# Kernel tuning notes

Hardware: AMD Instinct MI355X
Metric: run time of the kernel (lower is better)

Reference implementation:

```python
import jax, jax.numpy as jnp
import numpy as np

B, N, D, S, ITERS, EPS = 32, 4096, 512, 8, 3, 1e-8


def layer_norm(x, g, b, eps=1e-5):
    mu = jnp.mean(x, axis=-1, keepdims=True)
    var = jnp.var(x, axis=-1, keepdims=True)
    return (x - mu) * jax.lax.rsqrt(var + eps) * g + b


def setup_inputs() -> dict:
    key = jax.random.key(0)
    ks = jax.random.split(key, 12)
    sc = 1.0 / np.sqrt(D)
    return {
        "inputs": jax.random.normal(ks[0], (B, N, D), jnp.float32),
        "noise": jax.random.normal(ks[1], (B, S, D), jnp.float32),
        "slots_mu": jax.random.normal(ks[2], (1, S, D), jnp.float32),
        "slots_sigma": jnp.ones((1, S, D), jnp.float32),
        "ln_in_g": jnp.ones((D,), jnp.float32), "ln_in_b": jnp.zeros((D,), jnp.float32),
        "ln_s_g": jnp.ones((D,), jnp.float32), "ln_s_b": jnp.zeros((D,), jnp.float32),
        "wq": jax.random.normal(ks[3], (D, D), jnp.float32) * sc,
        "wk": jax.random.normal(ks[4], (D, D), jnp.float32) * sc,
        "wv": jax.random.normal(ks[5], (D, D), jnp.float32) * sc,
        "w_ih": jax.random.normal(ks[6], (3 * D, D), jnp.float32) * sc,
        "w_hh": jax.random.normal(ks[7], (3 * D, D), jnp.float32) * sc,
        "b_ih": jnp.zeros((3 * D,), jnp.float32),
        "b_hh": jnp.zeros((3 * D,), jnp.float32),
        "ln_m_g": jnp.ones((D,), jnp.float32), "ln_m_b": jnp.zeros((D,), jnp.float32),
        "w1": jax.random.normal(ks[8], (D, D), jnp.float32) * sc,
        "b1": jnp.zeros((D,), jnp.float32),
        "w2": jax.random.normal(ks[9], (D, D), jnp.float32) * sc,
        "b2": jnp.zeros((D,), jnp.float32),
    }


def reference(inputs, noise, slots_mu, slots_sigma, ln_in_g, ln_in_b, ln_s_g, ln_s_b,
              wq, wk, wv, w_ih, w_hh, b_ih, b_hh, ln_m_g, ln_m_b, w1, b1, w2, b2):
    # slot init: mu + sigma * N(0,1)
    slots = slots_mu + slots_sigma * noise          # (B,S,D)
    x = layer_norm(inputs, ln_in_g, ln_in_b)        # (B,N,D)
    k = jnp.einsum('bnd,ed->bne', x, wk)            # (B,N,D)
    v = jnp.einsum('bnd,ed->bne', x, wv)            # (B,N,D)
    for _ in range(ITERS):
        slots_prev = slots
        sn = layer_norm(slots, ln_s_g, ln_s_b)
        q = jnp.einsum('bsd,ed->bse', sn, wq)       # (B,S,D)
        logits = jnp.einsum('bnd,bsd->bns', k, q)   # (B,N,S)
        attn = jax.nn.softmax(logits, axis=-1) + EPS  # softmax over slots
        attn = attn / jnp.sum(attn, axis=-1, keepdims=True)
        attn_t = jnp.swapaxes(attn, -1, -2)         # (B,S,N)
        updates = jnp.einsum('bsn,bnd->bsd', attn_t, v)
        # GRUCell(input=updates, hidden=slots_prev)
        gi = jnp.einsum('bsd,ed->bse', updates, w_ih) + b_ih
        gh = jnp.einsum('bsd,ed->bse', slots_prev, w_hh) + b_hh
        gi_r, gi_z, gi_n = jnp.split(gi, 3, axis=-1)
        gh_r, gh_z, gh_n = jnp.split(gh, 3, axis=-1)
        r = jax.nn.sigmoid(gi_r + gh_r)
        z = jax.nn.sigmoid(gi_z + gh_z)
        n = jnp.tanh(gi_n + r * gh_n)
        slots = (1.0 - z) * n + z * slots_prev
        # residual MLP
        h = layer_norm(slots, ln_m_g, ln_m_b)
        h = jax.nn.relu(jnp.einsum('bsd,ed->bse', h, w1) + b1)
        slots = slots + jnp.einsum('bsd,ed->bse', h, w2) + b2
    return slots
```

## Files before the change

### kernel.cpp

```cpp
#include <hip/hip_runtime.h>

#define B_ 32
#define N_ 4096
#define D_ 512
#define S_ 8
#define ITERS_ 3

__device__ __forceinline__ float sigmoid_f(float x) {
    return 1.0f / (1.0f + __expf(-x));
}
__device__ __forceinline__ float tanh_f(float x) {
    float e = __expf(2.0f * x);
    return 1.0f - 2.0f / (e + 1.0f);
}

__global__ __launch_bounds__(256) void k_init(const float* __restrict__ noise,
                                              const float* __restrict__ mu,
                                              const float* __restrict__ sg,
                                              float* __restrict__ slots,
                                              float* __restrict__ stats) {
    int wid = threadIdx.x >> 6, lane = threadIdx.x & 63;
    int row = blockIdx.x * 4 + wid;
    const float4* nz = (const float4*)(noise + (size_t)row * D_);
    const float4* m4 = (const float4*)(mu + (size_t)(row & 7) * D_);
    const float4* s4 = (const float4*)(sg + (size_t)(row & 7) * D_);
    float4 v0 = nz[lane], v1 = nz[64 + lane];
    float4 a0 = m4[lane], a1 = m4[64 + lane];
    float4 c0 = s4[lane], c1 = s4[64 + lane];
    v0.x = fmaf(c0.x, v0.x, a0.x); v0.y = fmaf(c0.y, v0.y, a0.y);
    v0.z = fmaf(c0.z, v0.z, a0.z); v0.w = fmaf(c0.w, v0.w, a0.w);
    v1.x = fmaf(c1.x, v1.x, a1.x); v1.y = fmaf(c1.y, v1.y, a1.y);
    v1.z = fmaf(c1.z, v1.z, a1.z); v1.w = fmaf(c1.w, v1.w, a1.w);
    float4* o4 = (float4*)(slots + (size_t)row * D_);
    o4[lane] = v0; o4[64 + lane] = v1;
    float s1 = v0.x + v0.y + v0.z + v0.w + v1.x + v1.y + v1.z + v1.w;
    float s2 = v0.x*v0.x; s2 = fmaf(v0.y,v0.y,s2); s2 = fmaf(v0.z,v0.z,s2); s2 = fmaf(v0.w,v0.w,s2);
    s2 = fmaf(v1.x,v1.x,s2); s2 = fmaf(v1.y,v1.y,s2); s2 = fmaf(v1.z,v1.z,s2); s2 = fmaf(v1.w,v1.w,s2);
#pragma unroll
    for (int off = 32; off > 0; off >>= 1) {
        s1 += __shfl_xor(s1, off, 64);
        s2 += __shfl_xor(s2, off, 64);
    }
    if (lane == 0) {
        float mean = s1 * (1.0f / D_);
        float var  = s2 * (1.0f / D_) - mean * mean;
        stats[row * 2]     = mean;
        stats[row * 2 + 1] = rsqrtf(var + 1e-5f);
    }
}

template<int WT, int LNA>
__global__ __launch_bounds__(256) void k_gemm(const float* __restrict__ A,
                                              const float* __restrict__ W,
                                              const float* __restrict__ bias,
                                              float* __restrict__ C,
                                              int M, int N, int K,
                                              const float* __restrict__ stats,
                                              const float* __restrict__ lng,
                                              const float* __restrict__ lnb) {
    __shared__ float As[64][68];
    __shared__ float Ws[64][36];
    int t  = threadIdx.x;
    int bm = blockIdx.y * 64, bn = blockIdx.x * 32;
    int tm = t >> 4, tn = t & 15;
    float acc[4][2] = {{0.f,0.f},{0.f,0.f},{0.f,0.f},{0.f,0.f}};

    for (int kk = 0; kk < K; kk += 64) {
        __syncthreads();
        if (WT == 2) {
#pragma unroll
            for (int r = 0; r < 4; ++r) {
                int idx = t + r * 256;
                int k = idx >> 4, m4 = idx & 15;
                float4 a4 = *(const float4*)(A + (size_t)(kk + k) * M + bm + (m4 << 2));
                *(float4*)&As[k][m4 << 2] = a4;
            }
        } else {
#pragma unroll
            for (int r = 0; r < 4; ++r) {
                int flat = t * 4 + r * 1024;
                int m = flat >> 6, k = flat & 63;
                float4 a4 = *(const float4*)(A + (size_t)(bm + m) * K + kk + k);
                if (LNA) {
                    float mean = stats[(bm + m) * 2];
                    float rs   = stats[(bm + m) * 2 + 1];
                    float4 g4 = *(const float4*)(lng + kk + k);
                    float4 b4 = *(const float4*)(lnb + kk + k);
                    a4.x = fmaf((a4.x - mean) * rs, g4.x, b4.x);
                    a4.y = fmaf((a4.y - mean) * rs, g4.y, b4.y);
                    a4.z = fmaf((a4.z - mean) * rs, g4.z, b4.z);
                    a4.w = fmaf((a4.w - mean) * rs, g4.w, b4.w);
                }
                As[k + 0][m] = a4.x; As[k + 1][m] = a4.y;
                As[k + 2][m] = a4.z; As[k + 3][m] = a4.w;
            }
        }
        if (WT == 1) {
#pragma unroll
            for (int r = 0; r < 2; ++r) {
                int flat = t * 4 + r * 1024;
                int n = flat >> 6, k = flat & 63;
                float4 w4 = *(const float4*)(W + (size_t)(bn + n) * K + kk + k);
                Ws[k + 0][n] = w4.x; Ws[k + 1][n] = w4.y;
                Ws[k + 2][n] = w4.z; Ws[k + 3][n] = w4.w;
            }
        } else {
#pragma unroll
            for (int r = 0; r < 2; ++r) {
                int flat = t * 4 + r * 1024;
                int k = flat >> 5, n = flat & 31;
                float4 w4 = *(const float4*)(W + (size_t)(kk + k) * N + bn + n);
                *(float4*)&Ws[k][n] = w4;
            }
        }
        __syncthreads();
#pragma unroll
        for (int k = 0; k < 64; ++k) {
            float4 a = *(const float4*)&As[k][tm << 2];
            float2 w = *(const float2*)&Ws[k][tn << 1];
            acc[0][0] = fmaf(a.x, w.x, acc[0][0]); acc[0][1] = fmaf(a.x, w.y, acc[0][1]);
            acc[1][0] = fmaf(a.y, w.x, acc[1][0]); acc[1][1] = fmaf(a.y, w.y, acc[1][1]);
            acc[2][0] = fmaf(a.z, w.x, acc[2][0]); acc[2][1] = fmaf(a.z, w.y, acc[2][1]);
            acc[3][0] = fmaf(a.w, w.x, acc[3][0]); acc[3][1] = fmaf(a.w, w.y, acc[3][1]);
        }
    }
#pragma unroll
    for (int i = 0; i < 4; ++i) {
#pragma unroll
        for (int j = 0; j < 2; ++j) {
            int row = bm + (tm << 2) + i;
            int col = bn + (tn << 1) + j;
            float v = acc[i][j];
            if (bias) v += bias[col];
            C[(size_t)row * N + col] = v;
        }
    }
}

__global__ __launch_bounds__(512, 2) void k_attn_gh(const float* __restrict__ x,
                                                    const float* __restrict__ qk,
                                                    const float* __restrict__ g,
                                                    const float* __restrict__ bvec,
                                                    float* __restrict__ part,
                                                    float* __restrict__ bsum,
                                                    const float* __restrict__ slots,
                                                    const float* __restrict__ w_hh,
                                                    const float* __restrict__ b_hh,
                                                    float* __restrict__ gg) {
    __shared__ float smem[8704];
    const int blk = blockIdx.x;
    const int t = threadIdx.x;

    if (blk >= 512) {
        const int t2 = blk - 512;
        const int ci = t2 % 24, ri = t2 / 24;
        const int bm = ri * 64, bn = ci * 64;
        float (*As)[68] = (float (*)[68])smem;
        float (*Ws)[68] = (float (*)[68])(smem + 64 * 68);
        const int tm = t >> 5, tn = t & 31;
        float acc[4][2] = {{0.f,0.f},{0.f,0.f},{0.f,0.f},{0.f,0.f}};
        for (int kk = 0; kk < 512; kk += 64) {
            __syncthreads();
#pragma unroll
            for (int r = 0; r < 2; ++r) {
                int flat = t * 4 + r * 2048;
                int m = flat >> 6, k = flat & 63;
                float4 a4 = *(const float4*)(slots + (size_t)(bm + m) * 512 + kk + k);
                As[k + 0][m] = a4.x; As[k + 1][m] = a4.y;
                As[k + 2][m] = a4.z; As[k + 3][m] = a4.w;
            }
#pragma unroll
            for (int r = 0; r < 2; ++r) {
                int flat = t * 4 + r * 2048;
                int n = flat >> 6, k = flat & 63;
                float4 w4 = *(const float4*)(w_hh + (size_t)(bn + n) * 512 + kk + k);
                Ws[k + 0][n] = w4.x; Ws[k + 1][n] = w4.y;
                Ws[k + 2][n] = w4.z; Ws[k + 3][n] = w4.w;
            }
            __syncthreads();
#pragma unroll
            for (int k = 0; k < 64; ++k) {
                const float4 a = *(const float4*)&As[k][tm << 2];
                const float2 w = *(const float2*)&Ws[k][tn << 1];
                acc[0][0] = fmaf(a.x, w.x, acc[0][0]); acc[0][1] = fmaf(a.x, w.y, acc[0][1]);
                acc[1][0] = fmaf(a.y, w.x, acc[1][0]); acc[1][1] = fmaf(a.y, w.y, acc[1][1]);
                acc[2][0] = fmaf(a.z, w.x, acc[2][0]); acc[2][1] = fmaf(a.z, w.y, acc[2][1]);
                acc[3][0] = fmaf(a.w, w.x, acc[3][0]); acc[3][1] = fmaf(a.w, w.y, acc[3][1]);
            }
        }
#pragma unroll
        for (int i = 0; i < 4; ++i) {
#pragma unroll
            for (int j = 0; j < 2; ++j) {
                int row = bm + (tm << 2) + i;
                int col = bn + (tn << 1) + j;
                gg[(size_t)row * 3072 + col] = acc[i][j] + b_hh[col];
            }
        }
        return;
    }

    float* qts  = smem;
    float* u0s  = smem + 4096;
    float* red  = smem + 8192;
    float* red2 = smem + 8256;
    float* c12  = smem + 8320;
    const int nc = blk & 15, b = blk >> 4;
    const int w = t >> 6, lane = t & 63;

    {
        const float4* qk4 = (const float4*)(qk + (size_t)b * 4096);
        const float4* g4 = (const float4*)g;
        const float4* b4 = (const float4*)bvec;
        float c1p[2], c2p[2];
#pragma unroll
        for (int r = 0; r < 2; ++r) {
            int f = t + r * 512;
            float4 v = qk4[f];
            float4 gg4 = g4[f & 127];
            float4 bb = b4[f & 127];
            float4 qv = make_float4(v.x*gg4.x, v.y*gg4.y, v.z*gg4.z, v.w*gg4.w);
            *(float4*)&qts[((f & 127) * 8 + (f >> 7)) * 4] = qv;
            c1p[r] = qv.x + qv.y + qv.z + qv.w;
            c2p[r] = bb.x*v.x + bb.y*v.y + bb.z*v.z + bb.w*v.w;
        }
#pragma unroll
        for (int off = 32; off > 0; off >>= 1) {
#pragma unroll
            for (int r = 0; r < 2; ++r) {
                c1p[r] += __shfl_xor(c1p[r], off, 64);
                c2p[r] += __shfl_xor(c2p[r], off, 64);
            }
        }
        if (lane == 0) {
            red[w * 2 + 0] = c1p[0]; red[w * 2 + 1] = c1p[1];
            red2[w * 2 + 0] = c2p[0]; red2[w * 2 + 1] = c2p[1];
        }
    }
    __syncthreads();
    if (t < 8) {
        int s = t;
        float v1, v2;
        if (s < 4) { v1 = red[4*s]       + red[4*s + 2];       v2 = red2[4*s]       + red2[4*s + 2]; }
        else       { v1 = red[4*(s-4)+1] + red[4*(s-4)+3];     v2 = red2[4*(s-4)+1] + red2[4*(s-4)+3]; }
        c12[s] = v1; c12[8 + s] = v2;
    }
    __syncthreads();

    float4 qa[8], qb[8];
#pragma unroll
    for (int s = 0; s < 8; ++s) {
        qa[s] = *(const float4*)&qts[(lane * 8 + s) * 4];
        qb[s] = *(const float4*)&qts[((64 + lane) * 8 + s) * 4];
    }
    const int gq = (lane >> 3) & 7;
    const float c1g = c12[gq], c2g = c12[8 + gq];
    const bool hb5 = (lane & 32) != 0, hb4 = (lane & 16) != 0, hb3 = (lane & 8) != 0;
    const int gbase = lane & 7;
    const float cnorm = 1.0f / (1.0f + 8.0f * 1e-8f);
    const float eadd  = 1e-8f * cnorm;

    float4 acc0[8], acc1[8];
#pragma unroll
    for (int s = 0; s < 8; ++s) {
        acc0[s] = make_float4(0.f, 0.f, 0.f, 0.f);
        acc1[s] = make_float4(0.f, 0.f, 0.f, 0.f);
    }
    float aS = 0.f, tS = 0.f;

    const float4* xr = (const float4*)(x + ((size_t)b * N_ + (size_t)nc * 256 + w * 32) * D_);
    float4 cur0 = xr[lane],       cur1 = xr[64 + lane];
    float4 cur2 = xr[128 + lane], cur3 = xr[192 + lane];

#define DOTS(X0, X1, R)                                                          \
    {                                                                            \
        sx[R] = (X0).x + (X0).y + (X0).z + (X0).w                                \
              + (X1).x + (X1).y + (X1).z + (X1).w;                               \
        float t_ = (X0).x*(X0).x;                                                \
        t_ = fmaf((X0).y,(X0).y,t_); t_ = fmaf((X0).z,(X0).z,t_);                \
        t_ = fmaf((X0).w,(X0).w,t_); t_ = fmaf((X1).x,(X1).x,t_);                \
        t_ = fmaf((X1).y,(X1).y,t_); t_ = fmaf((X1).z,(X1).z,t_);                \
        t_ = fmaf((X1).w,(X1).w,t_); sxx[R] = t_;                                \
        _Pragma("unroll")                                                        \
        for (int s = 0; s < 8; ++s) {                                            \
            float td = (X0).x * qa[s].x;                                         \
            td = fmaf((X0).y, qa[s].y, td); td = fmaf((X0).z, qa[s].z, td);      \
            td = fmaf((X0).w, qa[s].w, td);                                      \
            td = fmaf((X1).x, qb[s].x, td); td = fmaf((X1).y, qb[s].y, td);      \
            td = fmaf((X1).z, qb[s].z, td); td = fmaf((X1).w, qb[s].w, td);      \
            dd[R][s] = td;                                                       \
        }                                                                        \
    }

    for (int jp = 0; jp < 16; ++jp) {
        int jn = (jp < 15) ? (2 * jp + 2) : 30;
        float4 n0 = xr[jn * 128 + lane],       n1 = xr[jn * 128 + 64 + lane];
        float4 n2 = xr[(jn + 1) * 128 + lane], n3 = xr[(jn + 1) * 128 + 64 + lane];

        float sx[2], sxx[2], dd[2][8];
        DOTS(cur0, cur1, 0);
        DOTS(cur2, cur3, 1);

        float r4[2][4];
#pragma unroll
        for (int r = 0; r < 2; ++r) {
#pragma unroll
            for (int s = 0; s < 4; ++s) {
                float snd = hb5 ? dd[r][s] : dd[r][s + 4];
                float kp  = hb5 ? dd[r][s + 4] : dd[r][s];
                r4[r][s] = kp + __shfl_xor(snd, 32, 64);
            }
        }
        float r2v[2][2];
#pragma unroll
        for (int r = 0; r < 2; ++r) {
#pragma unroll
            for (int s = 0; s < 2; ++s) {
                float snd = hb4 ? r4[r][s] : r4[r][s + 2];
                float kp  = hb4 ? r4[r][s + 2] : r4[r][s];
                r2v[r][s] = kp + __shfl_xor(snd, 16, 64);
            }
        }
        float vv[2];
#pragma unroll
        for (int r = 0; r < 2; ++r) {
            float snd = hb3 ? r2v[r][0] : r2v[r][1];
            float kp  = hb3 ? r2v[r][1] : r2v[r][0];
            vv[r] = kp + __shfl_xor(snd, 8, 64);
        }
#pragma unroll
        for (int off = 4; off > 0; off >>= 1) {
#pragma unroll
            for (int r = 0; r < 2; ++r) vv[r] += __shfl_xor(vv[r], off, 64);
        }
#pragma unroll
        for (int off = 32; off > 0; off >>= 1) {
#pragma unroll
            for (int r = 0; r < 2; ++r) {
                sx[r]  += __shfl_xor(sx[r], off, 64);
                sxx[r] += __shfl_xor(sxx[r], off, 64);
            }
        }
        float mean[2], rsv[2], lg[2];
#pragma unroll
        for (int r = 0; r < 2; ++r) {
            mean[r] = sx[r] * (1.0f / D_);
            rsv[r]  = rsqrtf(sxx[r] * (1.0f / D_) - mean[r] * mean[r] + 1e-5f);
            lg[r]   = fmaf(rsv[r], vv[r], fmaf(-rsv[r] * mean[r], c1g, c2g));
        }
        float mx[2] = { lg[0], lg[1] };
#pragma unroll
        for (int r = 0; r < 2; ++r) {
            mx[r] = fmaxf(mx[r], __shfl_xor(mx[r], 8, 64));
            mx[r] = fmaxf(mx[r], __shfl_xor(mx[r], 16, 64));
            mx[r] = fmaxf(mx[r], __shfl_xor(mx[r], 32, 64));
        }
        float pv[2], ps[2];
#pragma unroll
        for (int r = 0; r < 2; ++r) { pv[r] = __expf(lg[r] - mx[r]); ps[r] = pv[r]; }
#pragma unroll
        for (int r = 0; r < 2; ++r) {
            ps[r] += __shfl_xor(ps[r], 8, 64);
            ps[r] += __shfl_xor(ps[r], 16, 64);
            ps[r] += __shfl_xor(ps[r], 32, 64);
        }
        float av[2], wv[2];
#pragma unroll
        for (int r = 0; r < 2; ++r) {
            av[r] = fmaf(pv[r], cnorm / ps[r], eadd);
            wv[r] = av[r] * rsv[r];
        }
        aS += av[0]; aS += av[1];
        tS = fmaf(wv[0], mean[0], tS);
        tS = fmaf(wv[1], mean[1], tS);
#pragma unroll
        for (int s = 0; s < 8; ++s) {
            float w0 = __shfl(wv[0], (s << 3) | gbase, 64);
            float w1 = __shfl(wv[1], (s << 3) | gbase, 64);
            acc0[s].x = fmaf(w0, cur0.x, acc0[s].x); acc0[s].y = fmaf(w0, cur0.y, acc0[s].y);
            acc0[s].z = fmaf(w0, cur0.z, acc0[s].z); acc0[s].w = fmaf(w0, cur0.w, acc0[s].w);
            acc1[s].x = fmaf(w0, cur1.x, acc1[s].x); acc1[s].y = fmaf(w0, cur1.y, acc1[s].y);
            acc1[s].z = fmaf(w0, cur1.z, acc1[s].z); acc1[s].w = fmaf(w0, cur1.w, acc1[s].w);
            acc0[s].x = fmaf(w1, cur2.x, acc0[s].x); acc0[s].y = fmaf(w1, cur2.y, acc0[s].y);
            acc0[s].z = fmaf(w1, cur2.z, acc0[s].z); acc0[s].w = fmaf(w1, cur2.w, acc0[s].w);
            acc1[s].x = fmaf(w1, cur3.x, acc1[s].x); acc1[s].y = fmaf(w1, cur3.y, acc1[s].y);
            acc1[s].z = fmaf(w1, cur3.z, acc1[s].z); acc1[s].w = fmaf(w1, cur3.w, acc1[s].w);
        }
        cur0 = n0; cur1 = n1; cur2 = n2; cur3 = n3;
    }
#undef DOTS

    if ((lane & 7) == 0) { red[w * 8 + gq] = aS; red2[w * 8 + gq] = tS; }
    for (int w2 = 0; w2 < 8; ++w2) {
        if (w == w2) {
#pragma unroll
            for (int s = 0; s < 8; ++s) {
                float* p0 = &u0s[s * 512 + (lane << 2)];
                float* p1 = p0 + 256;
                if (w2 == 0) {
                    *(float4*)p0 = acc0[s];
                    *(float4*)p1 = acc1[s];
                } else {
                    float4 v0 = *(float4*)p0;
                    v0.x += acc0[s].x; v0.y += acc0[s].y; v0.z += acc0[s].z; v0.w += acc0[s].w;
                    *(float4*)p0 = v0;
                    float4 v1 = *(float4*)p1;
                    v1.x += acc1[s].x; v1.y += acc1[s].y; v1.z += acc1[s].z; v1.w += acc1[s].w;
                    *(float4*)p1 = v1;
                }
            }
        }
        __syncthreads();
    }
    if (t < 16) {
        int s = t & 7;
        const float* src = (t < 8) ? red : red2;
        float v = 0.f;
#pragma unroll
        for (int w2 = 0; w2 < 8; ++w2) v += src[w2 * 8 + s];
        bsum[(size_t)(b * 16 + nc) * 16 + t] = v;
    }
    float4* d4 = (float4*)(part + (size_t)(b * 16 + nc) * 4096);
    const float4* s4 = (const float4*)u0s;
    d4[t] = s4[t];
    d4[t + 512] = s4[t + 512];
}

__global__ __launch_bounds__(512) void k_ured(const float* __restrict__ part,
                                              const float* __restrict__ bsum,
                                              const float* __restrict__ g,
                                              const float* __restrict__ bvec,
                                              float* __restrict__ u0) {
    const int bs = blockIdx.x;
    const int b = bs >> 3, s = bs & 7;
    const int d = threadIdx.x;
    float Av = 0.f, Tv = 0.f;
#pragma unroll
    for (int nc = 0; nc < 16; ++nc) {
        Av += bsum[(size_t)(b * 16 + nc) * 16 + s];
        Tv += bsum[(size_t)(b * 16 + nc) * 16 + 8 + s];
    }
    float p = 0.f;
#pragma unroll
    for (int nc = 0; nc < 16; ++nc)
        p += part[(size_t)(b * 16 + nc) * 4096 + s * 512 + d];
    u0[(size_t)bs * 512 + d] = fmaf(g[d], p - Tv, Av * bvec[d]);
}

__global__ __launch_bounds__(256) void k_gi(const float* __restrict__ u0,
                                            const float* __restrict__ Wiv,
                                            const float* __restrict__ b_ih,
                                            float* __restrict__ gg) {
    __shared__ float As[64][68];
    __shared__ float Ws[64][36];
    const int t = threadIdx.x;
    const int bn = blockIdx.x * 32;
    const int bm = blockIdx.y * 64;
    int tm = t >> 4, tn = t & 15;
    float acc[4][2] = {{0.f,0.f},{0.f,0.f},{0.f,0.f},{0.f,0.f}};

    for (int kk = 0; kk < 512; kk += 64) {
        __syncthreads();
#pragma unroll
        for (int r = 0; r < 4; ++r) {
            int flat = t * 4 + r * 1024;
            int m = flat >> 6, k = flat & 63;
            float4 a4 = *(const float4*)(u0 + (size_t)(bm + m) * 512 + kk + k);
            As[k + 0][m] = a4.x; As[k + 1][m] = a4.y;
            As[k + 2][m] = a4.z; As[k + 3][m] = a4.w;
        }
#pragma unroll
        for (int r = 0; r < 2; ++r) {
            int flat = t * 4 + r * 1024;
            int n = flat >> 6, k = flat & 63;
            float4 w4 = *(const float4*)(Wiv + (size_t)(bn + n) * 512 + kk + k);
            Ws[k + 0][n] = w4.x; Ws[k + 1][n] = w4.y;
            Ws[k + 2][n] = w4.z; Ws[k + 3][n] = w4.w;
        }
        __syncthreads();
#pragma unroll
        for (int k = 0; k < 64; ++k) {
            float4 a = *(const float4*)&As[k][tm << 2];
            float2 w = *(const float2*)&Ws[k][tn << 1];
            acc[0][0] = fmaf(a.x, w.x, acc[0][0]); acc[0][1] = fmaf(a.x, w.y, acc[0][1]);
            acc[1][0] = fmaf(a.y, w.x, acc[1][0]); acc[1][1] = fmaf(a.y, w.y, acc[1][1]);
            acc[2][0] = fmaf(a.z, w.x, acc[2][0]); acc[2][1] = fmaf(a.z, w.y, acc[2][1]);
            acc[3][0] = fmaf(a.w, w.x, acc[3][0]); acc[3][1] = fmaf(a.w, w.y, acc[3][1]);
        }
    }
#pragma unroll
    for (int i = 0; i < 4; ++i) {
#pragma unroll
        for (int j = 0; j < 2; ++j) {
            int row = bm + (tm << 2) + i;
            int cw  = bn + (tn << 1) + j;
            gg[(size_t)row * 3072 + 1536 + cw] = acc[i][j] + b_ih[cw];
        }
    }
}

__global__ __launch_bounds__(512) void k_p2(const float* __restrict__ gg,
                                            const float* __restrict__ slots,
                                            const float* __restrict__ w1, const float* __restrict__ b1,
                                            const float* __restrict__ w2, const float* __restrict__ b2,
                                            const float* __restrict__ wqkT,
                                            const float* __restrict__ ln_m_g, const float* __restrict__ ln_m_b,
                                            const float* __restrict__ ln_s_g, const float* __restrict__ ln_s_b,
                                            float* __restrict__ dst, float* __restrict__ qkout, int last) {
    __shared__ float s2s[2][512];
    __shared__ float t0s[2][512];
    __shared__ float hs[2][512];
    __shared__ float stat[4];
    const int t = threadIdx.x;
    const int wid = t >> 6, lane = t & 63;
    const int r0 = blockIdx.x * 2;

#pragma unroll
    for (int j = 0; j < 2; ++j) {
        int flat = t + j * 512;
        int r = flat >> 9, d = flat & 511;
        size_t row = r0 + r;
        const float* ghb = gg + row * 3072;
        const float* gib = ghb + 1536;
        float gir = gib[d], giz = gib[d + 512], gin = gib[d + 1024];
        float ghr = ghb[d], ghz = ghb[d + 512], ghn = ghb[d + 1024];
        float rr = sigmoid_f(gir + ghr);
        float zz = sigmoid_f(giz + ghz);
        float nn = tanh_f(fmaf(rr, ghn, gin));
        float sp = slots[row * 512 + d];
        s2s[r][d] = fmaf(1.0f - zz, nn, zz * sp);
    }
    __syncthreads();
    if (wid < 2) {
        const float4* sr = (const float4*)s2s[wid];
        float4 a = sr[lane], bq = sr[64 + lane];
        float s1 = a.x + a.y + a.z + a.w + bq.x + bq.y + bq.z + bq.w;
        float s2 = a.x*a.x; s2 = fmaf(a.y,a.y,s2); s2 = fmaf(a.z,a.z,s2); s2 = fmaf(a.w,a.w,s2);
        s2 = fmaf(bq.x,bq.x,s2); s2 = fmaf(bq.y,bq.y,s2); s2 = fmaf(bq.z,bq.z,s2); s2 = fmaf(bq.w,bq.w,s2);
#pragma unroll
        for (int off = 32; off > 0; off >>= 1) {
            s1 += __shfl_xor(s1, off, 64);
            s2 += __shfl_xor(s2, off, 64);
        }
        if (lane == 0) {
            float mean = s1 * (1.0f / D_);
            float var  = s2 * (1.0f / D_) - mean * mean;
            stat[wid * 2] = mean;
            stat[wid * 2 + 1] = rsqrtf(var + 1e-5f);
        }
    }
    __syncthreads();
#pragma unroll
    for (int j = 0; j < 2; ++j) {
        int flat = t + j * 512;
        int r = flat >> 9, d = flat & 511;
        t0s[r][d] = fmaf((s2s[r][d] - stat[r * 2]) * stat[r * 2 + 1], ln_m_g[d], ln_m_b[d]);
    }
    __syncthreads();
    {
        const int c = t;
        const float4* wr = (const float4*)(w1 + (size_t)c * 512);
        float a0 = 0.f, a1 = 0.f;
#pragma unroll 8
        for (int k4 = 0; k4 < 128; ++k4) {
            float4 w4 = wr[k4];
            float4 q0 = *(const float4*)&t0s[0][k4 << 2];
            float4 q1 = *(const float4*)&t0s[1][k4 << 2];
            a0 = fmaf(q0.x, w4.x, a0); a0 = fmaf(q0.y, w4.y, a0);
            a0 = fmaf(q0.z, w4.z, a0); a0 = fmaf(q0.w, w4.w, a0);
            a1 = fmaf(q1.x, w4.x, a1); a1 = fmaf(q1.y, w4.y, a1);
            a1 = fmaf(q1.z, w4.z, a1); a1 = fmaf(q1.w, w4.w, a1);
        }
        float bc = b1[c];
        hs[0][c] = fmaxf(a0 + bc, 0.f);
        hs[1][c] = fmaxf(a1 + bc, 0.f);
    }
    __syncthreads();
    {
        const int c = t;
        const float4* wr = (const float4*)(w2 + (size_t)c * 512);
        float a0 = 0.f, a1 = 0.f;
#pragma unroll 8
        for (int k4 = 0; k4 < 128; ++k4) {
            float4 w4 = wr[k4];
            float4 q0 = *(const float4*)&hs[0][k4 << 2];
            float4 q1 = *(const float4*)&hs[1][k4 << 2];
            a0 = fmaf(q0.x, w4.x, a0); a0 = fmaf(q0.y, w4.y, a0);
            a0 = fmaf(q0.z, w4.z, a0); a0 = fmaf(q0.w, w4.w, a0);
            a1 = fmaf(q1.x, w4.x, a1); a1 = fmaf(q1.y, w4.y, a1);
            a1 = fmaf(q1.z, w4.z, a1); a1 = fmaf(q1.w, w4.w, a1);
        }
        float bc = b2[c];
        float o0 = s2s[0][c] + a0 + bc;
        float o1 = s2s[1][c] + a1 + bc;
        dst[(size_t)r0 * 512 + c] = o0;
        dst[(size_t)(r0 + 1) * 512 + c] = o1;
        s2s[0][c] = o0;
        s2s[1][c] = o1;
    }
    if (last) return;
    __syncthreads();
    if (wid < 2) {
        const float4* sr = (const float4*)s2s[wid];
        float4 a = sr[lane], bq = sr[64 + lane];
        float s1 = a.x + a.y + a.z + a.w + bq.x + bq.y + bq.z + bq.w;
        float s2 = a.x*a.x; s2 = fmaf(a.y,a.y,s2); s2 = fmaf(a.z,a.z,s2); s2 = fmaf(a.w,a.w,s2);
        s2 = fmaf(bq.x,bq.x,s2); s2 = fmaf(bq.y,bq.y,s2); s2 = fmaf(bq.z,bq.z,s2); s2 = fmaf(bq.w,bq.w,s2);
#pragma unroll
        for (int off = 32; off > 0; off >>= 1) {
            s1 += __shfl_xor(s1, off, 64);
            s2 += __shfl_xor(s2, off, 64);
        }
        if (lane == 0) {
            float mean = s1 * (1.0f / D_);
            float var  = s2 * (1.0f / D_) - mean * mean;
            stat[wid * 2] = mean;
            stat[wid * 2 + 1] = rsqrtf(var + 1e-5f);
        }
    }
    __syncthreads();
#pragma unroll
    for (int j = 0; j < 2; ++j) {
        int flat = t + j * 512;
        int r = flat >> 9, d = flat & 511;
        t0s[r][d] = fmaf((s2s[r][d] - stat[r * 2]) * stat[r * 2 + 1], ln_s_g[d], ln_s_b[d]);
    }
    __syncthreads();
    {
        const int c = t;
        const float4* wr = (const float4*)(wqkT + (size_t)c * 512);
        float a0 = 0.f, a1 = 0.f;
#pragma unroll 8
        for (int k4 = 0; k4 < 128; ++k4) {
            float4 w4 = wr[k4];
            float4 q0 = *(const float4*)&t0s[0][k4 << 2];
            float4 q1 = *(const float4*)&t0s[1][k4 << 2];
            a0 = fmaf(q0.x, w4.x, a0); a0 = fmaf(q0.y, w4.y, a0);
            a0 = fmaf(q0.z, w4.z, a0); a0 = fmaf(q0.w, w4.w, a0);
            a1 = fmaf(q1.x, w4.x, a1); a1 = fmaf(q1.y, w4.y, a1);
            a1 = fmaf(q1.z, w4.z, a1); a1 = fmaf(q1.w, w4.w, a1);
        }
        qkout[(size_t)r0 * 512 + c] = a0;
        qkout[(size_t)(r0 + 1) * 512 + c] = a1;
    }
}

extern "C" void kernel_launch(void* const* d_in, const int* in_sizes, int n_in,
                              void* d_out, int out_size, void* d_ws, size_t ws_size,
                              hipStream_t stream) {
    const float* inputs  = (const float*)d_in[0];
    const float* noise   = (const float*)d_in[1];
    const float* mu      = (const float*)d_in[2];
    const float* sg      = (const float*)d_in[3];
    const float* ln_in_g = (const float*)d_in[4];
    const float* ln_in_b = (const float*)d_in[5];
    const float* ln_s_g  = (const float*)d_in[6];
    const float* ln_s_b  = (const float*)d_in[7];
    const float* wq      = (const float*)d_in[8];
    const float* wk      = (const float*)d_in[9];
    const float* wv      = (const float*)d_in[10];
    const float* w_ih    = (const float*)d_in[11];
    const float* w_hh    = (const float*)d_in[12];
    const float* b_ih    = (const float*)d_in[13];
    const float* b_hh    = (const float*)d_in[14];
    const float* ln_m_g  = (const float*)d_in[15];
    const float* ln_m_b  = (const float*)d_in[16];
    const float* w1      = (const float*)d_in[17];
    const float* b1      = (const float*)d_in[18];
    const float* w2      = (const float*)d_in[19];
    const float* b2      = (const float*)d_in[20];

    float* ws = (float*)d_ws;
    const size_t SLOT = (size_t)B_ * S_ * D_;
    size_t o = 0;
    float* slots = ws + o; o += SLOT;
    float* qk    = ws + o; o += SLOT;
    float* u0    = ws + o; o += SLOT;
    float* gg    = ws + o; o += (size_t)256 * 3072;
    float* Mqk   = ws + o; o += (size_t)D_ * D_;
    float* Wiv   = ws + o; o += (size_t)3 * D_ * D_;
    float* statsS= ws + o; o += 512;
    float* part  = ws + o; o += (size_t)16 * B_ * 4096;
    float* bsum  = ws + o; o += (size_t)B_ * 16 * 16;

    k_gemm<2,0><<<dim3(16, 8), 256, 0, stream>>>(wk, wq, nullptr, Mqk,
                                                 512, 512, 512, nullptr, nullptr, nullptr);
    k_gemm<0,0><<<dim3(16, 24), 256, 0, stream>>>(w_ih, wv, nullptr, Wiv,
                                                  1536, 512, 512, nullptr, nullptr, nullptr);
    k_init<<<64, 256, 0, stream>>>(noise, mu, sg, slots, statsS);
    k_gemm<1,1><<<dim3(16, 4), 256, 0, stream>>>(slots, Mqk, nullptr, qk,
                                                 256, 512, 512, statsS, ln_s_g, ln_s_b);

    for (int it = 0; it < ITERS_; ++it) {
        k_attn_gh<<<608, 512, 0, stream>>>(inputs, qk, ln_in_g, ln_in_b, part, bsum,
                                           slots, w_hh, b_hh, gg);
        k_ured<<<256, 512, 0, stream>>>(part, bsum, ln_in_g, ln_in_b, u0);
        k_gi<<<dim3(48, 4), 256, 0, stream>>>(u0, Wiv, b_ih, gg);
        int last = (it == ITERS_ - 1);
        float* dst = last ? (float*)d_out : slots;
        k_p2<<<128, 512, 0, stream>>>(gg, slots, w1, b1, w2, b2, Mqk,
                                      ln_m_g, ln_m_b, ln_s_g, ln_s_b, dst, qk, last);
    }
}
```

Before: 700.4 us.

## Merge prologue kernels, cache input LN stats, restructure attention softmax via shared memory

Three prologue launches (two weight-product GEMMs and slot init) are merged into one kernel with a block-index dispatch. The attention kernel computes per-row layer-norm mean/rstd on the first iteration only, stores them to a workspace buffer, and reloads them in later iterations, so the sum and sum-of-squares reductions are not recomputed. The per-row softmax is also moved from shuffle-based cross-lane work to a single wave reading logits from shared memory, with 4 rows per warp per block step and extra block barriers. This adds a small workspace buffer and more synchronisation in exchange for fewer shuffles and launches.

```diff
diff --git a/kernel.cpp b/kernel.cpp
--- a/kernel.cpp
+++ b/kernel.cpp
@@ -14,54 +14,17 @@
     return 1.0f - 2.0f / (e + 1.0f);
 }
 
-__global__ __launch_bounds__(256) void k_init(const float* __restrict__ noise,
-                                              const float* __restrict__ mu,
-                                              const float* __restrict__ sg,
-                                              float* __restrict__ slots,
-                                              float* __restrict__ stats) {
-    int wid = threadIdx.x >> 6, lane = threadIdx.x & 63;
-    int row = blockIdx.x * 4 + wid;
-    const float4* nz = (const float4*)(noise + (size_t)row * D_);
-    const float4* m4 = (const float4*)(mu + (size_t)(row & 7) * D_);
-    const float4* s4 = (const float4*)(sg + (size_t)(row & 7) * D_);
-    float4 v0 = nz[lane], v1 = nz[64 + lane];
-    float4 a0 = m4[lane], a1 = m4[64 + lane];
-    float4 c0 = s4[lane], c1 = s4[64 + lane];
-    v0.x = fmaf(c0.x, v0.x, a0.x); v0.y = fmaf(c0.y, v0.y, a0.y);
-    v0.z = fmaf(c0.z, v0.z, a0.z); v0.w = fmaf(c0.w, v0.w, a0.w);
-    v1.x = fmaf(c1.x, v1.x, a1.x); v1.y = fmaf(c1.y, v1.y, a1.y);
-    v1.z = fmaf(c1.z, v1.z, a1.z); v1.w = fmaf(c1.w, v1.w, a1.w);
-    float4* o4 = (float4*)(slots + (size_t)row * D_);
-    o4[lane] = v0; o4[64 + lane] = v1;
-    float s1 = v0.x + v0.y + v0.z + v0.w + v1.x + v1.y + v1.z + v1.w;
-    float s2 = v0.x*v0.x; s2 = fmaf(v0.y,v0.y,s2); s2 = fmaf(v0.z,v0.z,s2); s2 = fmaf(v0.w,v0.w,s2);
-    s2 = fmaf(v1.x,v1.x,s2); s2 = fmaf(v1.y,v1.y,s2); s2 = fmaf(v1.z,v1.z,s2); s2 = fmaf(v1.w,v1.w,s2);
-#pragma unroll
-    for (int off = 32; off > 0; off >>= 1) {
-        s1 += __shfl_xor(s1, off, 64);
-        s2 += __shfl_xor(s2, off, 64);
-    }
-    if (lane == 0) {
-        float mean = s1 * (1.0f / D_);
-        float var  = s2 * (1.0f / D_) - mean * mean;
-        stats[row * 2]     = mean;
-        stats[row * 2 + 1] = rsqrtf(var + 1e-5f);
-    }
-}
-
 template<int WT, int LNA>
-__global__ __launch_bounds__(256) void k_gemm(const float* __restrict__ A,
-                                              const float* __restrict__ W,
-                                              const float* __restrict__ bias,
-                                              float* __restrict__ C,
-                                              int M, int N, int K,
-                                              const float* __restrict__ stats,
-                                              const float* __restrict__ lng,
-                                              const float* __restrict__ lnb) {
-    __shared__ float As[64][68];
-    __shared__ float Ws[64][36];
+__device__ void gemm_body(const float* __restrict__ A, const float* __restrict__ W,
+                          const float* __restrict__ bias, float* __restrict__ C,
+                          int M, int N, int K, int bxi, int byi,
+                          const float* __restrict__ stats,
+                          const float* __restrict__ lng, const float* __restrict__ lnb,
+                          float* smem) {
+    float (*As)[68] = (float (*)[68])smem;
+    float (*Ws)[36] = (float (*)[36])(smem + 64 * 68);
     int t  = threadIdx.x;
-    int bm = blockIdx.y * 64, bn = blockIdx.x * 32;
+    int bm = byi * 64, bn = bxi * 32;
     int tm = t >> 4, tn = t & 15;
     float acc[4][2] = {{0.f,0.f},{0.f,0.f},{0.f,0.f},{0.f,0.f}};
 
@@ -137,12 +100,77 @@
     }
 }
 
+__device__ void init_body(const float* __restrict__ noise, const float* __restrict__ mu,
+                          const float* __restrict__ sg, float* __restrict__ slots,
+                          float* __restrict__ stats, int blk) {
+    int wid = threadIdx.x >> 6, lane = threadIdx.x & 63;
+    int row = blk * 4 + wid;
+    const float4* nz = (const float4*)(noise + (size_t)row * D_);
+    const float4* m4 = (const float4*)(mu + (size_t)(row & 7) * D_);
+    const float4* s4 = (const float4*)(sg + (size_t)(row & 7) * D_);
+    float4 v0 = nz[lane], v1 = nz[64 + lane];
+    float4 a0 = m4[lane], a1 = m4[64 + lane];
+    float4 c0 = s4[lane], c1 = s4[64 + lane];
+    v0.x = fmaf(c0.x, v0.x, a0.x); v0.y = fmaf(c0.y, v0.y, a0.y);
+    v0.z = fmaf(c0.z, v0.z, a0.z); v0.w = fmaf(c0.w, v0.w, a0.w);
+    v1.x = fmaf(c1.x, v1.x, a1.x); v1.y = fmaf(c1.y, v1.y, a1.y);
+    v1.z = fmaf(c1.z, v1.z, a1.z); v1.w = fmaf(c1.w, v1.w, a1.w);
+    float4* o4 = (float4*)(slots + (size_t)row * D_);
+    o4[lane] = v0; o4[64 + lane] = v1;
+    float s1 = v0.x + v0.y + v0.z + v0.w + v1.x + v1.y + v1.z + v1.w;
+    float s2 = v0.x*v0.x; s2 = fmaf(v0.y,v0.y,s2); s2 = fmaf(v0.z,v0.z,s2); s2 = fmaf(v0.w,v0.w,s2);
+    s2 = fmaf(v1.x,v1.x,s2); s2 = fmaf(v1.y,v1.y,s2); s2 = fmaf(v1.z,v1.z,s2); s2 = fmaf(v1.w,v1.w,s2);
+#pragma unroll
+    for (int off = 32; off > 0; off >>= 1) {
+        s1 += __shfl_xor(s1, off, 64);
+        s2 += __shfl_xor(s2, off, 64);
+    }
+    if (lane == 0) {
+        float mean = s1 * (1.0f / D_);
+        float var  = s2 * (1.0f / D_) - mean * mean;
+        stats[row * 2]     = mean;
+        stats[row * 2 + 1] = rsqrtf(var + 1e-5f);
+    }
+}
+
+__global__ __launch_bounds__(256) void k_pro(const float* __restrict__ wk, const float* __restrict__ wq,
+                                             const float* __restrict__ w_ih, const float* __restrict__ wv,
+                                             float* __restrict__ Mqk, float* __restrict__ Wiv,
+                                             const float* __restrict__ noise, const float* __restrict__ mu,
+                                             const float* __restrict__ sg, float* __restrict__ slots,
+                                             float* __restrict__ stats) {
+    __shared__ float smem[64 * 68 + 64 * 36];
+    int blk = blockIdx.x;
+    if (blk < 128) {
+        gemm_body<2,0>(wk, wq, nullptr, Mqk, 512, 512, 512, blk & 15, blk >> 4,
+                       nullptr, nullptr, nullptr, smem);
+    } else if (blk < 512) {
+        int t2 = blk - 128;
+        gemm_body<0,0>(w_ih, wv, nullptr, Wiv, 1536, 512, 512, t2 & 15, t2 >> 4,
+                       nullptr, nullptr, nullptr, smem);
+    } else {
+        init_body(noise, mu, sg, slots, stats, blk - 512);
+    }
+}
+
+template<int WT, int LNA>
+__global__ __launch_bounds__(256) void k_gemm(const float* __restrict__ A, const float* __restrict__ W,
+                                              const float* __restrict__ bias, float* __restrict__ C,
+                                              int M, int N, int K,
+                                              const float* __restrict__ stats,
+                                              const float* __restrict__ lng, const float* __restrict__ lnb) {
+    __shared__ float smem[64 * 68 + 64 * 36];
+    gemm_body<WT,LNA>(A, W, bias, C, M, N, K, blockIdx.x, blockIdx.y, stats, lng, lnb, smem);
+}
+
+template<int FIRST>
 __global__ __launch_bounds__(512, 2) void k_attn_gh(const float* __restrict__ x,
                                                     const float* __restrict__ qk,
                                                     const float* __restrict__ g,
                                                     const float* __restrict__ bvec,
                                                     float* __restrict__ part,
                                                     float* __restrict__ bsum,
+                                                    float2* __restrict__ murs,
                                                     const float* __restrict__ slots,
                                                     const float* __restrict__ w_hh,
                                                     const float* __restrict__ b_hh,
@@ -201,12 +229,16 @@
     }
 
     float* qts  = smem;
-    float* u0s  = smem + 4096;
-    float* red  = smem + 8192;
-    float* red2 = smem + 8256;
-    float* c12  = smem + 8320;
+    float* dds  = smem + 4096;
+    float* wls  = smem + 4480;
+    float* mur  = smem + 4864;
+    float* redA = smem + 5376;
+    float* redB = smem + 5392;
+    float* c12  = smem + 5408;
+    float* u0s  = smem;
     const int nc = blk & 15, b = blk >> 4;
     const int w = t >> 6, lane = t & 63;
+    const size_t rowbase = (size_t)b * N_ + (size_t)nc * 256;
 
     {
         const float4* qk4 = (const float4*)(qk + (size_t)b * 4096);
@@ -233,16 +265,20 @@
             }
         }
         if (lane == 0) {
-            red[w * 2 + 0] = c1p[0]; red[w * 2 + 1] = c1p[1];
-            red2[w * 2 + 0] = c2p[0]; red2[w * 2 + 1] = c2p[1];
-        }
+            redA[w * 2 + 0] = c1p[0]; redA[w * 2 + 1] = c1p[1];
+            redB[w * 2 + 0] = c2p[0]; redB[w * 2 + 1] = c2p[1];
+        }
+    }
+    if (!FIRST && t < 256) {
+        float2 mm = murs[rowbase + t];
+        mur[2 * t] = mm.x; mur[2 * t + 1] = mm.y;
     }
     __syncthreads();
     if (t < 8) {
         int s = t;
         float v1, v2;
-        if (s < 4) { v1 = red[4*s]       + red[4*s + 2];       v2 = red2[4*s]       + red2[4*s + 2]; }
-        else       { v1 = red[4*(s-4)+1] + red[4*(s-4)+3];     v2 = red2[4*(s-4)+1] + red2[4*(s-4)+3]; }
+        if (s < 4) { v1 = redA[4*s]       + redA[4*s + 2];     v2 = redB[4*s]       + redB[4*s + 2]; }
+        else       { v1 = redA[4*(s-4)+1] + redA[4*(s-4)+3];   v2 = redB[4*(s-4)+1] + redB[4*(s-4)+3]; }
         c12[s] = v1; c12[8 + s] = v2;
     }
     __syncthreads();
@@ -253,10 +289,11 @@
         qa[s] = *(const float4*)&qts[(lane * 8 + s) * 4];
         qb[s] = *(const float4*)&qts[((64 + lane) * 8 + s) * 4];
     }
-    const int gq = (lane >> 3) & 7;
-    const float c1g = c12[gq], c2g = c12[8 + gq];
+    float c1r[8], c2r[8];
+#pragma unroll
+    for (int s = 0; s < 8; ++s) { c1r[s] = c12[s]; c2r[s] = c12[8 + s]; }
+
     const bool hb5 = (lane & 32) != 0, hb4 = (lane & 16) != 0, hb3 = (lane & 8) != 0;
-    const int gbase = lane & 7;
     const float cnorm = 1.0f / (1.0f + 8.0f * 1e-8f);
     const float eadd  = 1e-8f * cnorm;
 
@@ -266,131 +303,179 @@
         acc0[s] = make_float4(0.f, 0.f, 0.f, 0.f);
         acc1[s] = make_float4(0.f, 0.f, 0.f, 0.f);
     }
-    float aS = 0.f, tS = 0.f;
-
-    const float4* xr = (const float4*)(x + ((size_t)b * N_ + (size_t)nc * 256 + w * 32) * D_);
-    float4 cur0 = xr[lane],       cur1 = xr[64 + lane];
-    float4 cur2 = xr[128 + lane], cur3 = xr[192 + lane];
-
-#define DOTS(X0, X1, R)                                                          \
-    {                                                                            \
-        sx[R] = (X0).x + (X0).y + (X0).z + (X0).w                                \
-              + (X1).x + (X1).y + (X1).z + (X1).w;                               \
-        float t_ = (X0).x*(X0).x;                                                \
-        t_ = fmaf((X0).y,(X0).y,t_); t_ = fmaf((X0).z,(X0).z,t_);                \
-        t_ = fmaf((X0).w,(X0).w,t_); t_ = fmaf((X1).x,(X1).x,t_);                \
-        t_ = fmaf((X1).y,(X1).y,t_); t_ = fmaf((X1).z,(X1).z,t_);                \
-        t_ = fmaf((X1).w,(X1).w,t_); sxx[R] = t_;                                \
-        _Pragma("unroll")                                                        \
-        for (int s = 0; s < 8; ++s) {                                            \
-            float td = (X0).x * qa[s].x;                                         \
-            td = fmaf((X0).y, qa[s].y, td); td = fmaf((X0).z, qa[s].z, td);      \
-            td = fmaf((X0).w, qa[s].w, td);                                      \
-            td = fmaf((X1).x, qb[s].x, td); td = fmaf((X1).y, qb[s].y, td);      \
-            td = fmaf((X1).z, qb[s].z, td); td = fmaf((X1).w, qb[s].w, td);      \
-            dd[R][s] = td;                                                       \
-        }                                                                        \
-    }
-
-    for (int jp = 0; jp < 16; ++jp) {
-        int jn = (jp < 15) ? (2 * jp + 2) : 30;
-        float4 n0 = xr[jn * 128 + lane],       n1 = xr[jn * 128 + 64 + lane];
-        float4 n2 = xr[(jn + 1) * 128 + lane], n3 = xr[(jn + 1) * 128 + 64 + lane];
-
-        float sx[2], sxx[2], dd[2][8];
-        DOTS(cur0, cur1, 0);
-        DOTS(cur2, cur3, 1);
-
-        float r4[2][4];
-#pragma unroll
-        for (int r = 0; r < 2; ++r) {
+    float aS8[8] = {0,0,0,0,0,0,0,0}, tS8[8] = {0,0,0,0,0,0,0,0};
+
+    const float4* xg = (const float4*)(x + rowbase * D_);
+    float4 cur[8], nxt[8];
+    {
+        int r0 = w * 4;
+#pragma unroll
+        for (int i = 0; i < 4; ++i) {
+            cur[2*i]   = xg[(size_t)(r0 + i) * 128 + lane];
+            cur[2*i+1] = xg[(size_t)(r0 + i) * 128 + 64 + lane];
+        }
+    }
+
+    for (int jb = 0; jb < 8; ++jb) {
+#pragma unroll
+        for (int i = 0; i < 4; ++i) {
+            float4 xa = cur[2*i], xb = cur[2*i+1];
+            float dd[8];
+#pragma unroll
+            for (int s = 0; s < 8; ++s) {
+                float td = xa.x * qa[s].x;
+                td = fmaf(xa.y, qa[s].y, td); td = fmaf(xa.z, qa[s].z, td); td = fmaf(xa.w, qa[s].w, td);
+                td = fmaf(xb.x, qb[s].x, td); td = fmaf(xb.y, qb[s].y, td);
+                td = fmaf(xb.z, qb[s].z, td); td = fmaf(xb.w, qb[s].w, td);
+                dd[s] = td;
+            }
+            float r4[4];
 #pragma unroll
             for (int s = 0; s < 4; ++s) {
-                float snd = hb5 ? dd[r][s] : dd[r][s + 4];
-                float kp  = hb5 ? dd[r][s + 4] : dd[r][s];
-                r4[r][s] = kp + __shfl_xor(snd, 32, 64);
-            }
-        }
-        float r2v[2][2];
-#pragma unroll
-        for (int r = 0; r < 2; ++r) {
+                float snd = hb5 ? dd[s] : dd[s + 4];
+                float kp  = hb5 ? dd[s + 4] : dd[s];
+                r4[s] = kp + __shfl_xor(snd, 32, 64);
+            }
+            float r2v[2];
 #pragma unroll
             for (int s = 0; s < 2; ++s) {
-                float snd = hb4 ? r4[r][s] : r4[r][s + 2];
-                float kp  = hb4 ? r4[r][s + 2] : r4[r][s];
-                r2v[r][s] = kp + __shfl_xor(snd, 16, 64);
-            }
-        }
-        float vv[2];
-#pragma unroll
-        for (int r = 0; r < 2; ++r) {
-            float snd = hb3 ? r2v[r][0] : r2v[r][1];
-            float kp  = hb3 ? r2v[r][1] : r2v[r][0];
-            vv[r] = kp + __shfl_xor(snd, 8, 64);
-        }
-#pragma unroll
-        for (int off = 4; off > 0; off >>= 1) {
-#pragma unroll
-            for (int r = 0; r < 2; ++r) vv[r] += __shfl_xor(vv[r], off, 64);
-        }
+                float snd = hb4 ? r4[s] : r4[s + 2];
+                float kp  = hb4 ? r4[s + 2] : r4[s];
+                r2v[s] = kp + __shfl_xor(snd, 16, 64);
+            }
+            float v;
+            {
+                float snd = hb3 ? r2v[0] : r2v[1];
+                float kp  = hb3 ? r2v[1] : r2v[0];
+                v = kp + __shfl_xor(snd, 8, 64);
+            }
+            v += __shfl_xor(v, 4, 64);
+            v += __shfl_xor(v, 2, 64);
+            v += __shfl_xor(v, 1, 64);
+            int rb = w * 4 + i;
+            if ((lane & 7) == 0) dds[rb * 12 + (lane >> 3)] = v;
+
+            if (FIRST) {
+                float sx = xa.x + xa.y + xa.z + xa.w + xb.x + xb.y + xb.z + xb.w;
+                float sxx = xa.x*xa.x; sxx = fmaf(xa.y,xa.y,sxx); sxx = fmaf(xa.z,xa.z,sxx); sxx = fmaf(xa.w,xa.w,sxx);
+                sxx = fmaf(xb.x,xb.x,sxx); sxx = fmaf(xb.y,xb.y,sxx); sxx = fmaf(xb.z,xb.z,sxx); sxx = fmaf(xb.w,xb.w,sxx);
+#pragma unroll
+                for (int off = 32; off > 0; off >>= 1) {
+                    sx  += __shfl_xor(sx, off, 64);
+                    sxx += __shfl_xor(sxx, off, 64);
+                }
+                float mean = sx * (1.0f / D_);
+                float rs   = rsqrtf(sxx * (1.0f / D_) - mean * mean + 1e-5f);
+                if (lane == 0) {
+                    int br = jb * 32 + rb;
+                    mur[br * 2] = mean; mur[br * 2 + 1] = rs;
+                    murs[rowbase + br] = make_float2(mean, rs);
+                }
+            }
+        }
+        __syncthreads();
+        if (w == 0 && lane < 32) {
+            int br = jb * 32 + lane;
+            float4 d03 = *(const float4*)&dds[lane * 12];
+            float4 d47 = *(const float4*)&dds[lane * 12 + 4];
+            float mean = mur[br * 2], rs = mur[br * 2 + 1];
+            float mc = -rs * mean;
+            float lg[8];
+            lg[0] = fmaf(rs, d03.x, fmaf(mc, c1r[0], c2r[0]));
+            lg[1] = fmaf(rs, d03.y, fmaf(mc, c1r[1], c2r[1]));
+            lg[2] = fmaf(rs, d03.z, fmaf(mc, c1r[2], c2r[2]));
+            lg[3] = fmaf(rs, d03.w, fmaf(mc, c1r[3], c2r[3]));
+            lg[4] = fmaf(rs, d47.x, fmaf(mc, c1r[4], c2r[4]));
+            lg[5] = fmaf(rs, d47.y, fmaf(mc, c1r[5], c2r[5]));
+            lg[6] = fmaf(rs, d47.z, fmaf(mc, c1r[6], c2r[6]));
+            lg[7] = fmaf(rs, d47.w, fmaf(mc, c1r[7], c2r[7]));
+            float mx = lg[0];
+#pragma unroll
+            for (int s = 1; s < 8; ++s) mx = fmaxf(mx, lg[s]);
+            float p[8], psum = 0.f;
+#pragma unroll
+            for (int s = 0; s < 8; ++s) { p[s] = __expf(lg[s] - mx); psum += p[s]; }
+            float ip = cnorm / psum;
+            float wv[8];
+#pragma unroll
+            for (int s = 0; s < 8; ++s) {
+                float a = fmaf(p[s], ip, eadd);
+                wv[s] = a * rs;
+                aS8[s] += a;
+                tS8[s] = fmaf(wv[s], mean, tS8[s]);
+            }
+            *(float4*)&wls[lane * 12]     = make_float4(wv[0], wv[1], wv[2], wv[3]);
+            *(float4*)&wls[lane * 12 + 4] = make_float4(wv[4], wv[5], wv[6], wv[7]);
+        }
+        __syncthreads();
+        {
+            int jn = (jb < 7) ? jb + 1 : 7;
+            int r0 = jn * 32 + w * 4;
+#pragma unroll
+            for (int i = 0; i < 4; ++i) {
+                nxt[2*i]   = xg[(size_t)(r0 + i) * 128 + lane];
+                nxt[2*i+1] = xg[(size_t)(r0 + i) * 128 + 64 + lane];
+            }
+        }
+#pragma unroll
+        for (int i = 0; i < 4; ++i) {
+            int rb = w * 4 + i;
+            float4 w03 = *(const float4*)&wls[rb * 12];
+            float4 w47 = *(const float4*)&wls[rb * 12 + 4];
+            float4 xa = cur[2*i], xb = cur[2*i+1];
+            acc0[0].x = fmaf(w03.x, xa.x, acc0[0].x); acc0[0].y = fmaf(w03.x, xa.y, acc0[0].y);
+            acc0[0].z = fmaf(w03.x, xa.z, acc0[0].z); acc0[0].w = fmaf(w03.x, xa.w, acc0[0].w);
+            acc1[0].x = fmaf(w03.x, xb.x, acc1[0].x); acc1[0].y = fmaf(w03.x, xb.y, acc1[0].y);
+            acc1[0].z = fmaf(w03.x, xb.z, acc1[0].z); acc1[0].w = fmaf(w03.x, xb.w, acc1[0].w);
+            acc0[1].x = fmaf(w03.y, xa.x, acc0[1].x); acc0[1].y = fmaf(w03.y, xa.y, acc0[1].y);
+            acc0[1].z = fmaf(w03.y, xa.z, acc0[1].z); acc0[1].w = fmaf(w03.y, xa.w, acc0[1].w);
+            acc1[1].x = fmaf(w03.y, xb.x, acc1[1].x); acc1[1].y = fmaf(w03.y, xb.y, acc1[1].y);
+            acc1[1].z = fmaf(w03.y, xb.z, acc1[1].z); acc1[1].w = fmaf(w03.y, xb.w, acc1[1].w);
+            acc0[2].x = fmaf(w03.z, xa.x, acc0[2].x); acc0[2].y = fmaf(w03.z, xa.y, acc0[2].y);
+            acc0[2].z = fmaf(w03.z, xa.z, acc0[2].z); acc0[2].w = fmaf(w03.z, xa.w, acc0[2].w);
+            acc1[2].x = fmaf(w03.z, xb.x, acc1[2].x); acc1[2].y = fmaf(w03.z, xb.y, acc1[2].y);
+            acc1[2].z = fmaf(w03.z, xb.z, acc1[2].z); acc1[2].w = fmaf(w03.z, xb.w, acc1[2].w);
+            acc0[3].x = fmaf(w03.w, xa.x, acc0[3].x); acc0[3].y = fmaf(w03.w, xa.y, acc0[3].y);
+            acc0[3].z = fmaf(w03.w, xa.z, acc0[3].z); acc0[3].w = fmaf(w03.w, xa.w, acc0[3].w);
+            acc1[3].x = fmaf(w03.w, xb.x, acc1[3].x); acc1[3].y = fmaf(w03.w, xb.y, acc1[3].y);
+            acc1[3].z = fmaf(w03.w, xb.z, acc1[3].z); acc1[3].w = fmaf(w03.w, xb.w, acc1[3].w);
+            acc0[4].x = fmaf(w47.x, xa.x, acc0[4].x); acc0[4].y = fmaf(w47.x, xa.y, acc0[4].y);
+            acc0[4].z = fmaf(w47.x, xa.z, acc0[4].z); acc0[4].w = fmaf(w47.x, xa.w, acc0[4].w);
+            acc1[4].x = fmaf(w47.x, xb.x, acc1[4].x); acc1[4].y = fmaf(w47.x, xb.y, acc1[4].y);
+            acc1[4].z = fmaf(w47.x, xb.z, acc1[4].z); acc1[4].w = fmaf(w47.x, xb.w, acc1[4].w);
+            acc0[5].x = fmaf(w47.y, xa.x, acc0[5].x); acc0[5].y = fmaf(w47.y, xa.y, acc0[5].y);
+            acc0[5].z = fmaf(w47.y, xa.z, acc0[5].z); acc0[5].w = fmaf(w47.y, xa.w, acc0[5].w);
+            acc1[5].x = fmaf(w47.y, xb.x, acc1[5].x); acc1[5].y = fmaf(w47.y, xb.y, acc1[5].y);
+            acc1[5].z = fmaf(w47.y, xb.z, acc1[5].z); acc1[5].w = fmaf(w47.y, xb.w, acc1[5].w);
+            acc0[6].x = fmaf(w47.z, xa.x, acc0[6].x); acc0[6].y = fmaf(w47.z, xa.y, acc0[6].y);
+            acc0[6].z = fmaf(w47.z, xa.z, acc0[6].z); acc0[6].w = fmaf(w47.z, xa.w, acc0[6].w);
+            acc1[6].x = fmaf(w47.z, xb.x, acc1[6].x); acc1[6].y = fmaf(w47.z, xb.y, acc1[6].y);
+            acc1[6].z = fmaf(w47.z, xb.z, acc1[6].z); acc1[6].w = fmaf(w47.z, xb.w, acc1[6].w);
+            acc0[7].x = fmaf(w47.w, xa.x, acc0[7].x); acc0[7].y = fmaf(w47.w, xa.y, acc0[7].y);
+            acc0[7].z = fmaf(w47.w, xa.z, acc0[7].z); acc0[7].w = fmaf(w47.w, xa.w, acc0[7].w);
+            acc1[7].x = fmaf(w47.w, xb.x, acc1[7].x); acc1[7].y = fmaf(w47.w, xb.y, acc1[7].y);
+            acc1[7].z = fmaf(w47.w, xb.z, acc1[7].z); acc1[7].w = fmaf(w47.w, xb.w, acc1[7].w);
+        }
+#pragma unroll
+        for (int i = 0; i < 8; ++i) cur[i] = nxt[i];
+        __syncthreads();
+    }
+
+    if (w == 0) {
 #pragma unroll
         for (int off = 32; off > 0; off >>= 1) {
 #pragma unroll
-            for (int r = 0; r < 2; ++r) {
-                sx[r]  += __shfl_xor(sx[r], off, 64);
-                sxx[r] += __shfl_xor(sxx[r], off, 64);
-            }
-        }
-        float mean[2], rsv[2], lg[2];
-#pragma unroll
-        for (int r = 0; r < 2; ++r) {
-            mean[r] = sx[r] * (1.0f / D_);
-            rsv[r]  = rsqrtf(sxx[r] * (1.0f / D_) - mean[r] * mean[r] + 1e-5f);
-            lg[r]   = fmaf(rsv[r], vv[r], fmaf(-rsv[r] * mean[r], c1g, c2g));
-        }
-        float mx[2] = { lg[0], lg[1] };
-#pragma unroll
-        for (int r = 0; r < 2; ++r) {
-            mx[r] = fmaxf(mx[r], __shfl_xor(mx[r], 8, 64));
-            mx[r] = fmaxf(mx[r], __shfl_xor(mx[r], 16, 64));
-            mx[r] = fmaxf(mx[r], __shfl_xor(mx[r], 32, 64));
-        }
-        float pv[2], ps[2];
-#pragma unroll
-        for (int r = 0; r < 2; ++r) { pv[r] = __expf(lg[r] - mx[r]); ps[r] = pv[r]; }
-#pragma unroll
-        for (int r = 0; r < 2; ++r) {
-            ps[r] += __shfl_xor(ps[r], 8, 64);
-            ps[r] += __shfl_xor(ps[r], 16, 64);
-            ps[r] += __shfl_xor(ps[r], 32, 64);
-        }
-        float av[2], wv[2];
-#pragma unroll
-        for (int r = 0; r < 2; ++r) {
-            av[r] = fmaf(pv[r], cnorm / ps[r], eadd);
-            wv[r] = av[r] * rsv[r];
-        }
-        aS += av[0]; aS += av[1];
-        tS = fmaf(wv[0], mean[0], tS);
-        tS = fmaf(wv[1], mean[1], tS);
-#pragma unroll
-        for (int s = 0; s < 8; ++s) {
-            float w0 = __shfl(wv[0], (s << 3) | gbase, 64);
-            float w1 = __shfl(wv[1], (s << 3) | gbase, 64);
-            acc0[s].x = fmaf(w0, cur0.x, acc0[s].x); acc0[s].y = fmaf(w0, cur0.y, acc0[s].y);
-            acc0[s].z = fmaf(w0, cur0.z, acc0[s].z); acc0[s].w = fmaf(w0, cur0.w, acc0[s].w);
-            acc1[s].x = fmaf(w0, cur1.x, acc1[s].x); acc1[s].y = fmaf(w0, cur1.y, acc1[s].y);
-            acc1[s].z = fmaf(w0, cur1.z, acc1[s].z); acc1[s].w = fmaf(w0, cur1.w, acc1[s].w);
-            acc0[s].x = fmaf(w1, cur2.x, acc0[s].x); acc0[s].y = fmaf(w1, cur2.y, acc0[s].y);
-            acc0[s].z = fmaf(w1, cur2.z, acc0[s].z); acc0[s].w = fmaf(w1, cur2.w, acc0[s].w);
-            acc1[s].x = fmaf(w1, cur3.x, acc1[s].x); acc1[s].y = fmaf(w1, cur3.y, acc1[s].y);
-            acc1[s].z = fmaf(w1, cur3.z, acc1[s].z); acc1[s].w = fmaf(w1, cur3.w, acc1[s].w);
-        }
-        cur0 = n0; cur1 = n1; cur2 = n2; cur3 = n3;
-    }
-#undef DOTS
-
-    if ((lane & 7) == 0) { red[w * 8 + gq] = aS; red2[w * 8 + gq] = tS; }
+            for (int s = 0; s < 8; ++s) {
+                aS8[s] += __shfl_xor(aS8[s], off, 64);
+                tS8[s] += __shfl_xor(tS8[s], off, 64);
+            }
+        }
+        if (lane == 0) {
+            float* bs = bsum + (size_t)(b * 16 + nc) * 16;
+#pragma unroll
+            for (int s = 0; s < 8; ++s) { bs[s] = aS8[s]; bs[8 + s] = tS8[s]; }
+        }
+    }
     for (int w2 = 0; w2 < 8; ++w2) {
         if (w == w2) {
 #pragma unroll
@@ -411,14 +496,6 @@
             }
         }
         __syncthreads();
-    }
-    if (t < 16) {
-        int s = t & 7;
-        const float* src = (t < 8) ? red : red2;
-        float v = 0.f;
-#pragma unroll
-        for (int w2 = 0; w2 < 8; ++w2) v += src[w2 * 8 + s];
-        bsum[(size_t)(b * 16 + nc) * 16 + t] = v;
     }
     float4* d4 = (float4*)(part + (size_t)(b * 16 + nc) * 4096);
     const float4* s4 = (const float4*)u0s;
@@ -682,18 +759,19 @@
     float* statsS= ws + o; o += 512;
     float* part  = ws + o; o += (size_t)16 * B_ * 4096;
     float* bsum  = ws + o; o += (size_t)B_ * 16 * 16;
-
-    k_gemm<2,0><<<dim3(16, 8), 256, 0, stream>>>(wk, wq, nullptr, Mqk,
-                                                 512, 512, 512, nullptr, nullptr, nullptr);
-    k_gemm<0,0><<<dim3(16, 24), 256, 0, stream>>>(w_ih, wv, nullptr, Wiv,
-                                                  1536, 512, 512, nullptr, nullptr, nullptr);
-    k_init<<<64, 256, 0, stream>>>(noise, mu, sg, slots, statsS);
+    float2* murs = (float2*)(ws + o); o += (size_t)2 * B_ * N_;
+
+    k_pro<<<576, 256, 0, stream>>>(wk, wq, w_ih, wv, Mqk, Wiv, noise, mu, sg, slots, statsS);
     k_gemm<1,1><<<dim3(16, 4), 256, 0, stream>>>(slots, Mqk, nullptr, qk,
                                                  256, 512, 512, statsS, ln_s_g, ln_s_b);
 
     for (int it = 0; it < ITERS_; ++it) {
-        k_attn_gh<<<608, 512, 0, stream>>>(inputs, qk, ln_in_g, ln_in_b, part, bsum,
-                                           slots, w_hh, b_hh, gg);
+        if (it == 0)
+            k_attn_gh<1><<<608, 512, 0, stream>>>(inputs, qk, ln_in_g, ln_in_b, part, bsum,
+                                                  murs, slots, w_hh, b_hh, gg);
+        else
+            k_attn_gh<0><<<608, 512, 0, stream>>>(inputs, qk, ln_in_g, ln_in_b, part, bsum,
+                                                  murs, slots, w_hh, b_hh, gg);
         k_ured<<<256, 512, 0, stream>>>(part, bsum, ln_in_g, ln_in_b, u0);
         k_gi<<<dim3(48, 4), 256, 0, stream>>>(u0, Wiv, b_ih, gg);
         int last = (it == ITERS_ - 1);
```

Measured after the change: 693.6 us. No clear change (-1.0%).
